# Performance work log

Measured on AMD Instinct MI355X. Metric: run time of the kernel, lower is better.

The kernel has to match this reference:

```python
import jax, jax.numpy as jnp
import numpy as np

B, T, N, F = 8, 24, 207, 16
H = 64            # hidden_dim
DH = 16           # dims_hyper[-1] / node-embedding out
DA = 4 * F        # temporal attention dim_out
DS = 64           # ss_gal gcn out dim (last_ss_gal_dim)
GDEP = 2
ALPHA, BETA, GAMMA = 0.05, 0.95, 0.95
TA = 2.0


def _lin(x, w, b=None):
    y = x @ w
    return y if b is None else y + b


def gcn_hyper(x, A, W, b):
    # x: [B,N,C], A: [N,N] static. h <- a*x + g * einsum('nvc,vw->nwc', h, A)
    h = x
    outs = [h]
    for _ in range(GDEP):
        h = ALPHA * x + GAMMA * jnp.einsum('bvc,vw->bwc', h, A)
        outs.append(h)
    return _lin(jnp.concatenate(outs, axis=-1), W, b)


def gcn_gru(x, A_dyn, A_sta, W, b):
    # x: [B,N,C], A_dyn: [B,N,N], A_sta: [N,N]
    h = x
    outs = [h]
    for _ in range(GDEP):
        h = (ALPHA * x
             + BETA * jnp.einsum('bvw,bvc->bwc', A_dyn, h)     # bmm(A^T, h)
             + GAMMA * jnp.einsum('bvc,vw->bwc', h, A_sta))
        outs.append(h)
    return _lin(jnp.concatenate(outs, axis=-1), W, b)


def gcn_ssgal(x, A, W, b):
    # x: [B*,N,C], A: [B*,N,N]
    h = x
    outs = [h]
    for _ in range(GDEP):
        h = ALPHA * x + GAMMA * jnp.einsum('bvw,bvc->bwc', A, h)
        outs.append(h)
    return _lin(jnp.concatenate(outs, axis=-1), W, b)


def setup_inputs() -> dict:
    key = jax.random.key(0)
    ks = jax.random.split(key, 32)
    i = iter(range(32))
    w = lambda *s: (0.02 * jax.random.normal(ks[next(i)], s, dtype=jnp.float32))
    inp = {
        'input_sequence': jax.random.normal(ks[next(i)], (B, T, N, F), dtype=jnp.float32),
        'static_adj': jax.random.uniform(ks[next(i)], (N, N), dtype=jnp.float32),
        # hyper graph generators: mlp in = (GDEP+1)*H -> DH
        'src_gen_w': w((GDEP + 1) * H, DH), 'src_gen_b': w(DH),
        'tgt_gen_w': w((GDEP + 1) * H, DH), 'tgt_gen_b': w(DH),
        # node embeddings: F -> DH
        'src_emb_w': w(F, DH), 'src_emb_b': w(DH),
        'tgt_emb_w': w(F, DH), 'tgt_emb_b': w(DH),
        # GRU gate GCNs: mlp in = (GDEP+1)*(F+H) -> H
        'gru_z_w': w((GDEP + 1) * (F + H), H), 'gru_z_b': w(H),
        'gru_r_w': w((GDEP + 1) * (F + H), H), 'gru_r_b': w(H),
        'gru_c_w': w((GDEP + 1) * (F + H), H), 'gru_c_b': w(H),
        # temporal attention: F -> DA, score DA -> 1
        'attn_q_w': w(F, DA),
        'attn_k_w': w(F, DA), 'attn_k_b': w(DA),
        'attn_s_w': w(DA, 1),
        # ss_gal spatial gcn: (GDEP+1)*F -> DS
        'sgcn_w': w((GDEP + 1) * F, DS), 'sgcn_b': w(DS),
        # predictors
        'short_w': w(DS, F), 'short_b': w(F),
        'long_w': w(H, F), 'long_b': w(F),
        'fus_w': w(DS + H, F), 'fus_b': w(F),
    }
    return inp


def _forward(input_sequence, static_adj,
             src_gen_w, src_gen_b, tgt_gen_w, tgt_gen_b,
             src_emb_w, src_emb_b, tgt_emb_w, tgt_emb_b,
             gru_z_w, gru_z_b, gru_r_w, gru_r_b, gru_c_w, gru_c_b,
             attn_q_w, attn_k_w, attn_k_b, attn_s_w,
             sgcn_w, sgcn_b,
             short_w, short_b, long_w, long_b, fus_w, fus_b):
    batch, steps, nodes = input_sequence.shape[0], input_sequence.shape[1], input_sequence.shape[2]
    eye = jnp.eye(nodes, dtype=input_sequence.dtype)

    def cell(x_t, h):
        # x_t: [B,N,F], h: [B,N,H]
        src_ctx = gcn_hyper(h, static_adj, src_gen_w, src_gen_b)   # [B,N,DH]
        tgt_ctx = gcn_hyper(h, static_adj, tgt_gen_w, tgt_gen_b)
        s = jnp.tanh(TA * _lin(x_t, src_emb_w, src_emb_b) * src_ctx)
        t = jnp.tanh(TA * _lin(x_t, tgt_emb_w, tgt_emb_b) * tgt_ctx)
        asym = jnp.einsum('bnc,bmc->bnm', s, t) - jnp.einsum('bnc,bmc->bnm', t, s)
        adj = jax.nn.relu(jnp.tanh(TA * asym)) + eye
        adj = adj / (adj.sum(axis=-1, keepdims=True) + 1e-8)
        gi = jnp.concatenate([x_t, h], axis=-1)
        z = jax.nn.sigmoid(gcn_gru(gi, adj, static_adj, gru_z_w, gru_z_b))
        r = jax.nn.sigmoid(gcn_gru(gi, adj, static_adj, gru_r_w, gru_r_b))
        ri = jnp.concatenate([x_t, r * h], axis=-1)
        c = jnp.tanh(gcn_gru(ri, adj, static_adj, gru_c_w, gru_c_b))
        return z * h + (1.0 - z) * c

    h = jnp.zeros((batch, nodes, H), dtype=input_sequence.dtype)
    for t_step in range(0, max(1, steps - 4), 4):
        h = cell(input_sequence[:, t_step], h)

    # ss_gal branch on the last 4 steps
    recent = input_sequence[:, -4:]            # [B,4,N,F]
    target = input_sequence[:, -1]             # [B,N,F]
    # temporal attention
    q = target @ attn_q_w                      # [B,N,DA]
    k = recent @ attn_k_w + attn_k_b           # [B,4,N,DA]
    scores = jnp.tanh(q[:, None, :, None, :] + k[:, :, None, :, :])  # [B,4,N,N,DA]
    scores = jnp.squeeze(scores @ attn_s_w, axis=-1)                  # [B,4,N,N]
    attn = jax.nn.softmax(scores, axis=-1)
    dyn_adj = static_adj[None] + attn.reshape(-1, nodes, nodes)       # [B*4,N,N]
    rh = recent.reshape(-1, nodes, recent.shape[-1])                  # [B*4,N,F]
    rh = gcn_ssgal(rh, dyn_adj, sgcn_w, sgcn_b)                       # [B*4,N,DS]
    rh = jax.nn.relu(rh.reshape(batch, -1, nodes, rh.shape[-1]))      # [B,4,N,DS]
    target = jnp.sum(rh, axis=1)                                       # [B,N,DS]

    short = _lin(target, short_w, short_b)      # [B,N,F]
    h = cell(short, h)                          # final GRU step on short-term prediction
    long = _lin(h, long_w, long_b)              # [B,N,F]
    fused = _lin(jnp.concatenate([target, h], axis=-1), fus_w, fus_b)  # [B,N,F]
    return jnp.stack([short, long, fused], axis=0)  # [3,B,N,F]


def reference(input_sequence, static_adj,
              src_gen_w, src_gen_b, tgt_gen_w, tgt_gen_b,
              src_emb_w, src_emb_b, tgt_emb_w, tgt_emb_b,
              gru_z_w, gru_z_b, gru_r_w, gru_r_b, gru_c_w, gru_c_b,
              attn_q_w, attn_k_w, attn_k_b, attn_s_w,
              sgcn_w, sgcn_b,
              short_w, short_b, long_w, long_b, fus_w, fus_b):
    return _forward(input_sequence, static_adj,
                    src_gen_w, src_gen_b, tgt_gen_w, tgt_gen_b,
                    src_emb_w, src_emb_b, tgt_emb_w, tgt_emb_b,
                    gru_z_w, gru_z_b, gru_r_w, gru_r_b, gru_c_w, gru_c_b,
                    attn_q_w, attn_k_w, attn_k_b, attn_s_w,
                    sgcn_w, sgcn_b,
                    short_w, short_b, long_w, long_b, fus_w, fus_b)
```

## Files before the change

kernel.cpp:

```cpp
#include <hip/hip_runtime.h>


constexpr int B = 8, T = 24, N = 207, F = 16, H = 64, DH = 16;
constexpr int PS = 208;
constexpr float ALPHA = 0.05f, BETA = 0.95f, GAMMA = 0.95f, TA = 2.0f;
constexpr int NF = N * F;
constexpr int BNF = B * N * F;

__device__ __forceinline__ float tanh_fast(float x) { float e = __expf(2.f * x); return 1.f - 2.f / (e + 1.f); }
__device__ __forceinline__ float sigm(float x) { return 1.f / (1.f + __expf(-x)); }
__device__ __forceinline__ float tanh_pade(float x) {
    float x2 = x * x;
    float p = x * (27.f + x2);
    float q = 27.f + 9.f * x2;
    float r = p * __builtin_amdgcn_rcpf(q);
    return fminf(1.f, fmaxf(-1.f, r));
}

__global__ __launch_bounds__(256) void k_build_Ts(const float* __restrict__ adj, float* __restrict__ Ts) {
    int i = blockIdx.x * 256 + threadIdx.x;
    if (i >= N * N) return;
    int w = i / N, v = i % N;
    Ts[(size_t)w * PS + v] = adj[v * N + w];
}

__global__ __launch_bounds__(256) void k_mm_sq(const float* __restrict__ Ain, float* __restrict__ Aout) {
    int bb = blockIdx.z;
    const float* A = Ain + (size_t)bb * PS * PS;
    float* O = Aout + (size_t)bb * PS * PS;
    int w0 = blockIdx.x * 32, v0 = blockIdx.y * 32;
    int tid = threadIdx.x;
    __shared__ float sA[32][33], sB[32][33];
    float acc[4] = {0, 0, 0, 0};
    int i0 = tid >> 5, j = tid & 31;
    int r = tid >> 3, c4 = (tid & 7) * 4;
    for (int u0 = 0; u0 < N; u0 += 32) {
        float4 av = {0, 0, 0, 0}, bv = {0, 0, 0, 0};
        int w = w0 + r, u = u0 + r;
        if (w < N) av = *(const float4*)&A[(size_t)w * PS + u0 + c4];
        if (u < N) bv = *(const float4*)&A[(size_t)u * PS + v0 + c4];
        __syncthreads();
        sA[r][c4] = av.x; sA[r][c4 + 1] = av.y; sA[r][c4 + 2] = av.z; sA[r][c4 + 3] = av.w;
        sB[r][c4] = bv.x; sB[r][c4 + 1] = bv.y; sB[r][c4 + 2] = bv.z; sB[r][c4 + 3] = bv.w;
        __syncthreads();
#pragma unroll 8
        for (int u_ = 0; u_ < 32; u_++) {
            float bvv = sB[u_][j];
#pragma unroll
            for (int k = 0; k < 4; k++) acc[k] += sA[i0 + k * 8][u_] * bvv;
        }
    }
#pragma unroll
    for (int k = 0; k < 4; k++) {
        int w = w0 + i0 + k * 8, v = v0 + j;
        if (w < N && v < N) O[(size_t)w * PS + v] = acc[k];
    }
}

__global__ __launch_bounds__(256) void k_cell_a(
    const float* __restrict__ h, const float* __restrict__ Ts, const float* __restrict__ A2,
    const float* __restrict__ xseq, int tsel, const float* __restrict__ xbuf,
    const float* __restrict__ Wsrc, const float* __restrict__ bsrc,
    const float* __restrict__ Wtgt, const float* __restrict__ btgt,
    const float* __restrict__ Wes, const float* __restrict__ bes,
    const float* __restrict__ Wet, const float* __restrict__ bet,
    float* __restrict__ s_out, float* __restrict__ t_out, float* __restrict__ catg) {
    int b = blockIdx.y, w0 = blockIdx.x * 16;
    int tid = threadIdx.x, ty = tid >> 4, tx = tid & 15;
    __shared__ float sTs[16][33], sA2[16][33];
    __shared__ float sH[32][64];
    __shared__ float cat[16][193];
    __shared__ float sW[192][16];
    __shared__ float sX[16][16], sWe[16][16];
    float au[4] = {0, 0, 0, 0}, aw[4] = {0, 0, 0, 0};
    const float* hb = h + b * N * H;
    const float* xp = (tsel >= 0) ? (xseq + ((size_t)(b * T + tsel)) * NF) : (xbuf + (size_t)b * NF);
    int pidx = tid & 127;
    int pr = pidx >> 3, pc4 = (pidx & 7) * 4;
    for (int v0 = 0; v0 < N; v0 += 32) {
        float4 t4 = {0, 0, 0, 0};
        {
            const float* src = (tid < 128) ? Ts : A2;
            int w = w0 + pr;
            if (w < N) t4 = *(const float4*)&src[(size_t)w * PS + v0 + pc4];
        }
        float4 h4[2];
        int hr[2], hc[2];
#pragma unroll
        for (int k = 0; k < 2; k++) {
            int l4 = tid + k * 256;
            hr[k] = l4 >> 4; hc[k] = (l4 & 15) * 4;
            float4 hv = {0, 0, 0, 0};
            int v = v0 + hr[k];
            if (v < N) hv = *(const float4*)&hb[(size_t)v * H + hc[k]];
            h4[k] = hv;
        }
        __syncthreads();
        {
            float (*dst)[33] = (tid < 128) ? sTs : sA2;
            dst[pr][pc4] = t4.x; dst[pr][pc4 + 1] = t4.y; dst[pr][pc4 + 2] = t4.z; dst[pr][pc4 + 3] = t4.w;
        }
#pragma unroll
        for (int k = 0; k < 2; k++) *(float4*)&sH[hr[k]][hc[k]] = h4[k];
        __syncthreads();
#pragma unroll 8
        for (int v = 0; v < 32; v++) {
            float pu = sTs[ty][v], pw = sA2[ty][v];
#pragma unroll
            for (int j = 0; j < 4; j++) {
                float x = sH[v][tx * 4 + j];
                au[j] += pu * x; aw[j] += pw * x;
            }
        }
    }
    int w = w0 + ty;
    bool valid = w < N;
    __syncthreads();
    if (valid) {
#pragma unroll
        for (int j = 0; j < 4; j++) {
            int c = tx * 4 + j;
            float hv = hb[w * H + c];
            float u = au[j], w2 = aw[j];
            cat[ty][c] = hv;
            cat[ty][64 + c] = ALPHA * hv + GAMMA * u;
            cat[ty][128 + c] = ALPHA * hv + ALPHA * GAMMA * u + GAMMA * GAMMA * w2;
        }
    } else {
#pragma unroll
        for (int j = 0; j < 4; j++) {
            int c = tx * 4 + j;
            cat[ty][c] = 0; cat[ty][64 + c] = 0; cat[ty][128 + c] = 0;
        }
    }
    {
        float4 wv[3];
#pragma unroll
        for (int k = 0; k < 3; k++) {
            int l4 = tid + k * 256;
            wv[k] = *(const float4*)&Wsrc[l4 * 4];
        }
        float4 xv = {0, 0, 0, 0}, ev = {0, 0, 0, 0};
        int sr = 0, sc = 0;
        if (tid < 64) {
            sr = tid >> 2; sc = (tid & 3) * 4;
            int n = w0 + sr;
            if (n < N) xv = *(const float4*)&xp[(size_t)n * F + sc];
            ev = *(const float4*)&Wes[tid * 4];
        }
#pragma unroll
        for (int k = 0; k < 3; k++) {
            int l4 = tid + k * 256;
            int r = l4 >> 2, c4 = (l4 & 3) * 4;
            *(float4*)&sW[r][c4] = wv[k];
        }
        if (tid < 64) {
            *(float4*)&sX[sr][sc] = xv;
            *(float4*)&sWe[sr][sc] = ev;
        }
    }
    __syncthreads();
    if (valid) {
#pragma unroll
        for (int j = 0; j < 5; j++) {
            int c = tx * 5 + j;
            float v = (c < 16) ? sX[ty][c] : hb[w * H + (c - 16)];
            catg[((size_t)(b * N + w)) * 240 + c] = v;
        }
    }
    {
        float ctx = bsrc[tx];
#pragma unroll 8
        for (int c = 0; c < 192; c++) ctx += cat[ty][c] * sW[c][tx];
        float xe = bes[tx];
#pragma unroll
        for (int f = 0; f < 16; f++) xe += sX[ty][f] * sWe[f][tx];
        if (valid) s_out[(b * N + w) * DH + tx] = tanh_fast(TA * xe * ctx);
    }
    __syncthreads();
    {
        float4 wv[3];
#pragma unroll
        for (int k = 0; k < 3; k++) {
            int l4 = tid + k * 256;
            wv[k] = *(const float4*)&Wtgt[l4 * 4];
        }
        float4 ev = {0, 0, 0, 0};
        if (tid < 64) ev = *(const float4*)&Wet[tid * 4];
#pragma unroll
        for (int k = 0; k < 3; k++) {
            int l4 = tid + k * 256;
            int r = l4 >> 2, c4 = (l4 & 3) * 4;
            *(float4*)&sW[r][c4] = wv[k];
        }
        if (tid < 64) *(float4*)&sWe[tid >> 2][(tid & 3) * 4] = ev;
    }
    __syncthreads();
    {
        float ctx = btgt[tx];
#pragma unroll 8
        for (int c = 0; c < 192; c++) ctx += cat[ty][c] * sW[c][tx];
        float xe = bet[tx];
#pragma unroll
        for (int f = 0; f < 16; f++) xe += sX[ty][f] * sWe[f][tx];
        if (valid) t_out[(b * N + w) * DH + tx] = tanh_fast(TA * xe * ctx);
    }
}

__global__ __launch_bounds__(256) void k_cell_bP(const float* __restrict__ s_in, const float* __restrict__ t_in,
                                                 const float* __restrict__ adj, float* __restrict__ P) {
    int b = blockIdx.y, v0 = blockIdx.x * 16;
    int tid = threadIdx.x, ty = tid >> 4, tx = tid & 15;
    __shared__ float sS[N][17], sT[N][17];
    for (int l4 = tid; l4 < 828; l4 += 256) {
        float4 sv = *(const float4*)&s_in[(size_t)b * N * 16 + l4 * 4];
        float4 tv = *(const float4*)&t_in[(size_t)b * N * 16 + l4 * 4];
        int r = l4 >> 2, c = (l4 & 3) * 4;
        sS[r][c] = sv.x; sS[r][c + 1] = sv.y; sS[r][c + 2] = sv.z; sS[r][c + 3] = sv.w;
        sT[r][c] = tv.x; sT[r][c + 1] = tv.y; sT[r][c + 2] = tv.z; sT[r][c + 3] = tv.w;
    }
    __syncthreads();
    int v = v0 + ty;
    bool valid = v < N;
    int vc = valid ? v : (N - 1);
    float sv[16], tv[16];
#pragma unroll
    for (int k = 0; k < 16; k++) { sv[k] = sS[vc][k]; tv[k] = sT[vc][k]; }
    float val[13];
    float rsum = 0.f;
#pragma unroll
    for (int idx = 0; idx < 13; idx++) {
        int w = tx + 16 * idx;
        float r = 0.f;
        if (w < N) {
            float a = 0.f;
#pragma unroll
            for (int k = 0; k < 16; k++) a += sv[k] * sT[w][k] - tv[k] * sS[w][k];
            r = tanh_fast(TA * a);
            r = r > 0.f ? r : 0.f;
            if (w == v) r += 1.f;
        }
        val[idx] = r;
        rsum += r;
    }
    float tot = rsum;
    for (int d = 8; d > 0; d >>= 1) tot += __shfl_down(tot, d, 16);
    tot = __shfl(tot, 0, 16);
    float rinv = BETA / (tot + 1e-8f);
    if (valid) {
        float* Pb = P + (size_t)b * PS * PS;
#pragma unroll
        for (int idx = 0; idx < 13; idx++) {
            int w = tx + 16 * idx;
            if (w < N) Pb[(size_t)w * PS + v] = val[idx] * rinv + GAMMA * adj[v * N + w];
        }
    }
}

__global__ __launch_bounds__(256) void k_combineT(const float* __restrict__ Ain, const float* __restrict__ rs,
                                                  const float* __restrict__ Ts, float* __restrict__ Pout,
                                                  float cA, float cT) {
    int bt = blockIdx.z;
    int w0 = blockIdx.x * 32, v0 = blockIdx.y * 32;
    int tid = threadIdx.x;
    __shared__ float tile[32][33];
    __shared__ float rsv[32];
    int r = tid >> 3, c4 = (tid & 7) * 4;
    float4 a4 = {0, 0, 0, 0};
    int v = v0 + r;
    if (v < N) a4 = *(const float4*)&Ain[(size_t)bt * PS * PS + (size_t)v * PS + w0 + c4];
    tile[r][c4] = a4.x; tile[r][c4 + 1] = a4.y; tile[r][c4 + 2] = a4.z; tile[r][c4 + 3] = a4.w;
    if (tid < 32) {
        int vv = v0 + tid;
        rsv[tid] = (vv < N) ? (cA / rs[bt * N + vv]) : 0.f;
    }
    __syncthreads();
    for (int l = tid; l < 1024; l += 256) {
        int i = l >> 5, j = l & 31;
        int w = w0 + i, vv = v0 + j;
        if (w < N && vv < N)
            Pout[(size_t)bt * PS * PS + (size_t)w * PS + vv] = tile[j][i] * rsv[j] + cT * Ts[(size_t)w * PS + vv];
    }
}

__global__ __launch_bounds__(256) void k_prop2(const float* __restrict__ P, const float* __restrict__ P2,
                                               float* __restrict__ cat) {
    int b = blockIdx.y, w0 = blockIdx.x * 16, c0 = blockIdx.z * 16;
    int tid = threadIdx.x, ty = tid >> 4, tx = tid & 15;
    const float* Pb = P + (size_t)b * PS * PS;
    const float* P2b = P2 + (size_t)b * PS * PS;
    __shared__ float sP[16][33], sP2[16][33], sX[32][17];
    float a1 = 0.f, a2 = 0.f;
    int pr = tid >> 4, pc = (tid & 15) * 2;
    int xr = tid >> 3, xc = (tid & 7) * 2;
    for (int v0 = 0; v0 < N; v0 += 32) {
        float2 pv = {0, 0}, p2v = {0, 0}, xv = {0, 0};
        int w = w0 + pr;
        if (w < N) {
            pv = *(const float2*)&Pb[(size_t)w * PS + v0 + pc];
            p2v = *(const float2*)&P2b[(size_t)w * PS + v0 + pc];
        }
        int vv = v0 + xr;
        if (vv < N) xv = *(const float2*)&cat[((size_t)(b * N + vv)) * 240 + c0 + xc];
        __syncthreads();
        sP[pr][pc] = pv.x; sP[pr][pc + 1] = pv.y;
        sP2[pr][pc] = p2v.x; sP2[pr][pc + 1] = p2v.y;
        sX[xr][xc] = xv.x; sX[xr][xc + 1] = xv.y;
        __syncthreads();
#pragma unroll 8
        for (int v_ = 0; v_ < 32; v_++) {
            float xx = sX[v_][tx];
            a1 += sP[ty][v_] * xx;
            a2 += sP2[ty][v_] * xx;
        }
    }
    int w = w0 + ty, c = c0 + tx;
    if (w < N) {
        size_t base = ((size_t)(b * N + w)) * 240;
        float x0 = cat[base + c];
        cat[base + 80 + c] = ALPHA * x0 + a1;
        cat[base + 160 + c] = ALPHA * x0 + ALPHA * a1 + a2;
    }
}

__global__ __launch_bounds__(256) void k_gate(
    const float* __restrict__ cat,
    const float* __restrict__ Wa, const float* __restrict__ ba,
    const float* __restrict__ Wb, const float* __restrict__ bb,
    int baseMode,
    const float* __restrict__ xseq, int tsel, const float* __restrict__ xbuf,
    float* __restrict__ zbuf, float* __restrict__ ricat,
    float* __restrict__ h,
    const float* __restrict__ target,
    const float* __restrict__ Wlong, const float* __restrict__ blong,
    const float* __restrict__ Wfus, const float* __restrict__ bfus,
    float* __restrict__ out) {
    int mode = baseMode + blockIdx.z;
    const float* W = (mode == 1) ? Wb : Wa;
    const float* bias = (mode == 1) ? bb : ba;
    int b = blockIdx.y, w0 = blockIdx.x * 16;
    int tid = threadIdx.x, ty = tid >> 4, tx = tid & 15;
    __shared__ float sC[16][241];
    __shared__ float sW[48][65];
    __shared__ float hrow[16][65], trow[16][65];
    for (int l4 = tid; l4 < 960; l4 += 256) {
        int r = l4 / 60, cc = (l4 % 60) * 4;
        int w = w0 + r;
        float4 v4 = {0, 0, 0, 0};
        if (w < N) v4 = *(const float4*)&cat[((size_t)(b * N + w)) * 240 + cc];
        sC[r][cc] = v4.x; sC[r][cc + 1] = v4.y; sC[r][cc + 2] = v4.z; sC[r][cc + 3] = v4.w;
    }
    float acc[4];
#pragma unroll
    for (int j = 0; j < 4; j++) acc[j] = bias[tx * 4 + j];
    for (int c0 = 0; c0 < 240; c0 += 48) {
        float4 wv[3];
#pragma unroll
        for (int k = 0; k < 3; k++) {
            int l4 = tid + k * 256;
            wv[k] = *(const float4*)&W[(size_t)c0 * 64 + l4 * 4];
        }
        __syncthreads();
#pragma unroll
        for (int k = 0; k < 3; k++) {
            int l4 = tid + k * 256;
            int r = l4 >> 4, cc = (l4 & 15) * 4;
            sW[r][cc] = wv[k].x; sW[r][cc + 1] = wv[k].y; sW[r][cc + 2] = wv[k].z; sW[r][cc + 3] = wv[k].w;
        }
        __syncthreads();
#pragma unroll 8
        for (int cc = 0; cc < 48; cc++) {
            float cv = sC[ty][c0 + cc];
#pragma unroll
            for (int j = 0; j < 4; j++) acc[j] += cv * sW[cc][tx * 4 + j];
        }
    }
    int w = w0 + ty;
    bool valid = w < N;
    if (mode == 0) {
        if (valid) {
#pragma unroll
            for (int j = 0; j < 4; j++) zbuf[((size_t)(b * N + w)) * 64 + tx * 4 + j] = sigm(acc[j]);
        }
    } else if (mode == 1) {
        if (valid) {
#pragma unroll
            for (int j = 0; j < 4; j++) {
                int o = tx * 4 + j;
                ricat[((size_t)(b * N + w)) * 240 + 16 + o] = sigm(acc[j]) * h[((size_t)(b * N + w)) * 64 + o];
            }
            if (tx < 4) {
                const float* xp = (tsel >= 0) ? (xseq + ((size_t)(b * T + tsel)) * NF) : (xbuf + (size_t)b * NF);
#pragma unroll
                for (int j = 0; j < 4; j++) {
                    int c = tx * 4 + j;
                    ricat[((size_t)(b * N + w)) * 240 + c] = xp[w * F + c];
                }
            }
        }
    } else {
#pragma unroll
        for (int j = 0; j < 4; j++) {
            int o = tx * 4 + j;
            float cval = tanh_fast(acc[j]);
            float zv = 0.f, hv = 0.f;
            if (valid) { zv = zbuf[((size_t)(b * N + w)) * 64 + o]; hv = h[((size_t)(b * N + w)) * 64 + o]; }
            float hn = zv * hv + (1.f - zv) * cval;
            if (valid) h[((size_t)(b * N + w)) * 64 + o] = hn;
            hrow[ty][o] = valid ? hn : 0.f;
        }
        if (mode == 3) {
            for (int l = tid; l < 1024; l += 256) {
                int i = l >> 6, o = l & 63;
                int ww = w0 + i;
                trow[i][o] = (ww < N) ? target[((size_t)(b * N + ww)) * 64 + o] : 0.f;
            }
            __syncthreads();
            float lg = blong[tx];
            float fs = bfus[tx];
            for (int o = 0; o < 64; o++) {
                lg += hrow[ty][o] * Wlong[o * 16 + tx];
                fs += trow[ty][o] * Wfus[o * 16 + tx] + hrow[ty][o] * Wfus[(64 + o) * 16 + tx];
            }
            if (valid) {
                out[((size_t)1 * B * N + b * N + w) * 16 + tx] = lg;
                out[((size_t)2 * B * N + b * N + w) * 16 + tx] = fs;
            }
        }
    }
}

__global__ __launch_bounds__(256) void k_qk(const float* __restrict__ inp,
                                            const float* __restrict__ Wq,
                                            const float* __restrict__ Wk,
                                            const float* __restrict__ kb,
                                            float* __restrict__ q, float* __restrict__ kkk) {
    int b = blockIdx.z, which = blockIdx.y, n0 = blockIdx.x * 16;
    int tid = threadIdx.x, ty = tid >> 4, tx = tid & 15;
    __shared__ float sX[16][16], sW[16][64];
    int tsel = (which == 0) ? (T - 1) : (T - 4 + which - 1);
    const float* W = (which == 0) ? Wq : Wk;
    {
        float4 wv = *(const float4*)&W[tid * 4];
        float4 xv = {0, 0, 0, 0};
        if (tid < 64) {
            int r = tid >> 2, c4 = (tid & 3) * 4;
            int n = n0 + r;
            if (n < N) xv = *(const float4*)&inp[((size_t)(b * T + tsel) * N + n) * F + c4];
            *(float4*)&sX[r][c4] = xv;
        }
        *(float4*)&sW[tid >> 4][(tid & 15) * 4] = wv;
    }
    __syncthreads();
    float acc[4];
#pragma unroll
    for (int j = 0; j < 4; j++) {
        int o = tx * 4 + j;
        float a = (which == 0) ? 0.f : kb[o];
        for (int f = 0; f < 16; f++) a += sX[ty][f] * sW[f][o];
        acc[j] = a;
    }
    int n = n0 + ty;
    if (n < N) {
        float* dst = (which == 0) ? (q + (b * N + n) * 64) : (kkk + ((b * 4 + (which - 1)) * N + n) * 64);
#pragma unroll
        for (int j = 0; j < 4; j++) dst[tx * 4 + j] = acc[j];
    }
}

__global__ __launch_bounds__(256) void k_attn2(const float* __restrict__ q, const float* __restrict__ kkk,
                                               const float* __restrict__ sw_,
                                               float* __restrict__ attnU, float* __restrict__ rsum) {
    int bt = blockIdx.z, b = bt >> 2;
    int n0 = blockIdx.x * 16, m0 = blockIdx.y * 16;
    int tid = threadIdx.x, ti = tid >> 4, tj = tid & 15;
    __shared__ float sQ[16][65], sK[16][65], ssw[64];
    {
        int r = tid >> 4, c4 = (tid & 15) * 4;
        int n = n0 + r, m = m0 + r;
        float4 qv = {0, 0, 0, 0}, kv = {0, 0, 0, 0};
        if (n < N) qv = *(const float4*)&q[((size_t)(b * N + n)) * 64 + c4];
        if (m < N) kv = *(const float4*)&kkk[((size_t)(bt * N + m)) * 64 + c4];
        sQ[r][c4] = qv.x; sQ[r][c4 + 1] = qv.y; sQ[r][c4 + 2] = qv.z; sQ[r][c4 + 3] = qv.w;
        sK[r][c4] = kv.x; sK[r][c4 + 1] = kv.y; sK[r][c4 + 2] = kv.z; sK[r][c4 + 3] = kv.w;
    }
    if (tid < 64) ssw[tid] = sw_[tid];
    __syncthreads();
    float sc = 0.f;
#pragma unroll 4
    for (int d = 0; d < 64; d++) sc += tanh_pade(sQ[ti][d] + sK[tj][d]) * ssw[d];
    int n = n0 + ti, m = m0 + tj;
    bool vn = n < N, vm = m < N;
    float e = (vn && vm) ? __expf(sc) : 0.f;
    float part = e;
    for (int d = 8; d > 0; d >>= 1) part += __shfl_down(part, d, 16);
    if (tj == 0 && vn) atomicAdd(&rsum[bt * N + n], part);
    if (vn && vm) attnU[(size_t)bt * PS * PS + (size_t)n * PS + m] = e;
}

__global__ __launch_bounds__(256) void k_prop_xr(const float* __restrict__ Pd, const float* __restrict__ inp,
                                                 float* __restrict__ x1) {
    int bt = blockIdx.y, w0 = blockIdx.x * 16;
    int b = bt >> 2, tau = bt & 3;
    const float* xb = inp + ((size_t)(b * T + 20 + tau)) * NF;
    const float* Pb = Pd + (size_t)bt * PS * PS;
    int tid = threadIdx.x, ty = tid >> 4, tx = tid & 15;
    __shared__ float sP[16][33];
    __shared__ float sX[32][17];
    float acc = 0.f;
    for (int v0 = 0; v0 < N; v0 += 32) {
        float4 pv = {0, 0, 0, 0}, xv = {0, 0, 0, 0};
        if (tid < 128) {
            int r = tid >> 3, c4 = (tid & 7) * 4;
            int w = w0 + r;
            if (w < N) pv = *(const float4*)&Pb[(size_t)w * PS + v0 + c4];
        } else {
            int idx = tid - 128;
            int r = idx >> 2, c4 = (idx & 3) * 4;
            int v = v0 + r;
            if (v < N) xv = *(const float4*)&xb[(size_t)v * F + c4];
        }
        __syncthreads();
        if (tid < 128) {
            int r = tid >> 3, c4 = (tid & 7) * 4;
            sP[r][c4] = pv.x; sP[r][c4 + 1] = pv.y; sP[r][c4 + 2] = pv.z; sP[r][c4 + 3] = pv.w;
        } else {
            int idx = tid - 128;
            int r = idx >> 2, c4 = (idx & 3) * 4;
            sX[r][c4] = xv.x; sX[r][c4 + 1] = xv.y; sX[r][c4 + 2] = xv.z; sX[r][c4 + 3] = xv.w;
        }
        __syncthreads();
#pragma unroll 8
        for (int v = 0; v < 32; v++) acc += sP[ty][v] * sX[v][tx];
    }
    int w = w0 + ty;
    if (w < N) x1[((size_t)(bt * N + w)) * 16 + tx] = ALPHA * xb[w * F + tx] + acc;
}

__global__ __launch_bounds__(256) void k_sgc2(const float* __restrict__ Pd, const float* __restrict__ x1,
                                              const float* __restrict__ inp,
                                              const float* __restrict__ Ws, const float* __restrict__ bs,
                                              float* __restrict__ target) {
    int bt = blockIdx.y, b = bt >> 2, tau = bt & 3, w0 = blockIdx.x * 16;
    const float* xb = inp + ((size_t)(b * T + 20 + tau)) * NF;
    const float* Pb = Pd + (size_t)bt * PS * PS;
    int tid = threadIdx.x, ty = tid >> 4, tx = tid & 15;
    __shared__ float sP[16][33], sX[32][17], cat[16][48], sW[48][64];
    float acc = 0.f;
    for (int v0 = 0; v0 < N; v0 += 32) {
        float4 pv = {0, 0, 0, 0}, xv = {0, 0, 0, 0};
        if (tid < 128) {
            int r = tid >> 3, c4 = (tid & 7) * 4;
            int w = w0 + r;
            if (w < N) pv = *(const float4*)&Pb[(size_t)w * PS + v0 + c4];
        } else {
            int idx = tid - 128;
            int r = idx >> 2, c4 = (idx & 3) * 4;
            int v = v0 + r;
            if (v < N) xv = *(const float4*)&x1[((size_t)(bt * N + v)) * 16 + c4];
        }
        __syncthreads();
        if (tid < 128) {
            int r = tid >> 3, c4 = (tid & 7) * 4;
            sP[r][c4] = pv.x; sP[r][c4 + 1] = pv.y; sP[r][c4 + 2] = pv.z; sP[r][c4 + 3] = pv.w;
        } else {
            int idx = tid - 128;
            int r = idx >> 2, c4 = (idx & 3) * 4;
            sX[r][c4] = xv.x; sX[r][c4 + 1] = xv.y; sX[r][c4 + 2] = xv.z; sX[r][c4 + 3] = xv.w;
        }
        __syncthreads();
#pragma unroll 8
        for (int v = 0; v < 32; v++) acc += sP[ty][v] * sX[v][tx];
    }
    int w = w0 + ty;
    bool valid = w < N;
    __syncthreads();
    for (int l = tid; l < 512; l += 256) {
        int i = l >> 5, c = l & 31;
        int ww = w0 + i;
        float vv = 0;
        if (ww < N) {
            if (c < 16) vv = xb[ww * F + c];
            else vv = x1[((size_t)bt * N + ww) * 16 + (c - 16)];
        }
        cat[i][c] = vv;
    }
    {
        float x0 = valid ? xb[w * F + tx] : 0.f;
        cat[ty][32 + tx] = ALPHA * x0 + acc;
    }
    {
        float4 wv[3];
#pragma unroll
        for (int k = 0; k < 3; k++) wv[k] = *(const float4*)&Ws[(tid + k * 256) * 4];
#pragma unroll
        for (int k = 0; k < 3; k++) {
            int l4 = tid + k * 256;
            *(float4*)&sW[l4 >> 4][(l4 & 15) * 4] = wv[k];
        }
    }
    __syncthreads();
    float a[4];
#pragma unroll
    for (int j = 0; j < 4; j++) a[j] = bs[tx * 4 + j];
#pragma unroll 8
    for (int cc = 0; cc < 48; cc++) {
        float cv = cat[ty][cc];
#pragma unroll
        for (int j = 0; j < 4; j++) a[j] += cv * sW[cc][tx * 4 + j];
    }
    if (valid) {
#pragma unroll
        for (int j = 0; j < 4; j++) {
            float r = a[j] > 0.f ? a[j] : 0.f;
            atomicAdd(&target[(b * N + w) * 64 + tx * 4 + j], r);
        }
    }
}

__global__ __launch_bounds__(256) void k_short(const float* __restrict__ target,
                                               const float* __restrict__ Wsh, const float* __restrict__ bsh,
                                               float* __restrict__ out, float* __restrict__ xshort) {
    int b = blockIdx.y, n0 = blockIdx.x * 16;
    int tid = threadIdx.x, ty = tid >> 4, tx = tid & 15;
    __shared__ float trow[16][65], sW[64][16];
    {
        int r = tid >> 4, c4 = (tid & 15) * 4;
        int n = n0 + r;
        float4 tv = {0, 0, 0, 0};
        if (n < N) tv = *(const float4*)&target[((size_t)(b * N + n)) * 64 + c4];
        trow[r][c4] = tv.x; trow[r][c4 + 1] = tv.y; trow[r][c4 + 2] = tv.z; trow[r][c4 + 3] = tv.w;
        float4 wv = *(const float4*)&Wsh[tid * 4];
        *(float4*)&sW[tid >> 2][(tid & 3) * 4] = wv;
    }
    __syncthreads();
    float a = bsh[tx];
#pragma unroll 8
    for (int o = 0; o < 64; o++) a += trow[ty][o] * sW[o][tx];
    int n = n0 + ty;
    if (n < N) {
        out[((size_t)0 * B * N + b * N + n) * 16 + tx] = a;
        xshort[(b * N + n) * 16 + tx] = a;
    }
}

extern "C" void kernel_launch(void* const* d_in, const int* in_sizes, int n_in,
                              void* d_out, int out_size, void* d_ws, size_t ws_size,
                              hipStream_t stream) {
    const float* inp = (const float*)d_in[0];
    const float* adj = (const float*)d_in[1];
    const float* src_gen_w = (const float*)d_in[2];
    const float* src_gen_b = (const float*)d_in[3];
    const float* tgt_gen_w = (const float*)d_in[4];
    const float* tgt_gen_b = (const float*)d_in[5];
    const float* src_emb_w = (const float*)d_in[6];
    const float* src_emb_b = (const float*)d_in[7];
    const float* tgt_emb_w = (const float*)d_in[8];
    const float* tgt_emb_b = (const float*)d_in[9];
    const float* gru_z_w = (const float*)d_in[10];
    const float* gru_z_b = (const float*)d_in[11];
    const float* gru_r_w = (const float*)d_in[12];
    const float* gru_r_b = (const float*)d_in[13];
    const float* gru_c_w = (const float*)d_in[14];
    const float* gru_c_b = (const float*)d_in[15];
    const float* attn_q_w = (const float*)d_in[16];
    const float* attn_k_w = (const float*)d_in[17];
    const float* attn_k_b = (const float*)d_in[18];
    const float* attn_s_w = (const float*)d_in[19];
    const float* sgcn_w = (const float*)d_in[20];
    const float* sgcn_b = (const float*)d_in[21];
    const float* short_w = (const float*)d_in[22];
    const float* short_b = (const float*)d_in[23];
    const float* long_w = (const float*)d_in[24];
    const float* long_b = (const float*)d_in[25];
    const float* fus_w = (const float*)d_in[26];
    const float* fus_b = (const float*)d_in[27];
    float* out = (float*)d_out;

    float* ws = (float*)d_ws;
    size_t off = 0;
    auto A = [&](size_t n) { n = (n + 3) & ~(size_t)3; float* p = ws + off; off += n; return p; };
    float* Ts = A((size_t)PS * PS);
    float* A2 = A((size_t)PS * PS);
    float* h = A((size_t)B * N * H);
    float* sbuf = A((size_t)B * N * DH);
    float* tbuf = A((size_t)B * N * DH);
    float* P = A((size_t)B * PS * PS);
    float* P2 = A((size_t)B * PS * PS);
    float* catg = A((size_t)B * N * 240);
    float* catc = A((size_t)B * N * 240);
    float* zb = A((size_t)B * N * 64);
    float* q = A((size_t)B * N * 64);
    float* kk = A((size_t)B * 4 * N * 64);
    float* attnU = A((size_t)32 * PS * PS);
    float* Pd = A((size_t)32 * PS * PS);
    float* x1 = A((size_t)32 * NF);
    float* target = A((size_t)B * N * 64);
    float* rsum = A((size_t)32 * N);
    float* xshort = A(BNF);
    (void)ws_size; (void)in_sizes; (void)n_in; (void)out_size;

    hipMemsetAsync(h, 0, sizeof(float) * B * N * H, stream);
    hipMemsetAsync(target, 0, sizeof(float) * (B * N * 64), stream);
    hipMemsetAsync(rsum, 0, sizeof(float) * (32 * N), stream);
    k_build_Ts<<<(N * N + 255) / 256, 256, 0, stream>>>(adj, Ts);
    k_mm_sq<<<dim3(7, 7, 1), 256, 0, stream>>>(Ts, A2);

    auto run_cell = [&](int tsel, const float* xbuf, int finalFlag) {
        k_cell_a<<<dim3(13, B), 256, 0, stream>>>(h, Ts, A2, inp, tsel, xbuf,
                                                  src_gen_w, src_gen_b, tgt_gen_w, tgt_gen_b,
                                                  src_emb_w, src_emb_b, tgt_emb_w, tgt_emb_b, sbuf, tbuf, catg);
        k_cell_bP<<<dim3(13, B), 256, 0, stream>>>(sbuf, tbuf, adj, P);
        k_mm_sq<<<dim3(7, 7, B), 256, 0, stream>>>(P, P2);
        k_prop2<<<dim3(13, B, 5), 256, 0, stream>>>(P, P2, catg);
        k_gate<<<dim3(13, B, 2), 256, 0, stream>>>(catg, gru_z_w, gru_z_b, gru_r_w, gru_r_b, 0,
                                                   inp, tsel, xbuf, zb, catc, h,
                                                   nullptr, nullptr, nullptr, nullptr, nullptr, nullptr);
        k_prop2<<<dim3(13, B, 5), 256, 0, stream>>>(P, P2, catc);
        k_gate<<<dim3(13, B, 1), 256, 0, stream>>>(catc, gru_c_w, gru_c_b, nullptr, nullptr, 2 + finalFlag,
                                                   nullptr, 0, nullptr, zb, nullptr, h,
                                                   target, long_w, long_b, fus_w, fus_b, out);
    };

    for (int t = 0; t < 20; t += 4) run_cell(t, nullptr, 0);

    k_qk<<<dim3(13, 5, B), 256, 0, stream>>>(inp, attn_q_w, attn_k_w, attn_k_b, q, kk);
    k_attn2<<<dim3(13, 13, 32), 256, 0, stream>>>(q, kk, attn_s_w, attnU, rsum);
    k_combineT<<<dim3(7, 7, 32), 256, 0, stream>>>(attnU, rsum, Ts, Pd, GAMMA, GAMMA);
    k_prop_xr<<<dim3(13, 32), 256, 0, stream>>>(Pd, inp, x1);
    k_sgc2<<<dim3(13, 32), 256, 0, stream>>>(Pd, x1, inp, sgcn_w, sgcn_b, target);
    k_short<<<dim3(13, B), 256, 0, stream>>>(target, short_w, short_b, out, xshort);

    run_cell(-1, xshort, 1);
}
```

Before: 728.0 us.

## Double-buffer shared-memory tiles in GEMM-like kernels and fuse Q/K projection into attention

Converts the tiled loops in k_mm_sq, k_cell_a, k_prop2, k_gate, k_prop_xr and k_sgc2 to double-buffered shared memory. Each thread issues the global loads for the next tile before computing on the current one, so load latency overlaps with the FMA loop. It also drops the separate k_qk launch and its q/kk buffers by computing the Q and K projections inside k_attn2 from the input. This removes one launch and a global round trip, but recomputes the projections redundantly in each attention block and increases LDS use per block.

```diff
diff --git a/kernel.cpp b/kernel.cpp
--- a/kernel.cpp
+++ b/kernel.cpp
@@ -28,31 +28,38 @@
     int bb = blockIdx.z;
     const float* A = Ain + (size_t)bb * PS * PS;
     float* O = Aout + (size_t)bb * PS * PS;
-    int w0 = blockIdx.x * 32, v0 = blockIdx.y * 32;
+    int w0 = blockIdx.x * 32, v0b = blockIdx.y * 32;
     int tid = threadIdx.x;
-    __shared__ float sA[32][33], sB[32][33];
+    __shared__ float sA[2][32][33], sB[2][32][33];
     float acc[4] = {0, 0, 0, 0};
     int i0 = tid >> 5, j = tid & 31;
     int r = tid >> 3, c4 = (tid & 7) * 4;
-    for (int u0 = 0; u0 < N; u0 += 32) {
-        float4 av = {0, 0, 0, 0}, bv = {0, 0, 0, 0};
+    float4 av, bv;
+    auto loadT = [&](int u0) {
+        av = make_float4(0, 0, 0, 0); bv = make_float4(0, 0, 0, 0);
         int w = w0 + r, u = u0 + r;
         if (w < N) av = *(const float4*)&A[(size_t)w * PS + u0 + c4];
-        if (u < N) bv = *(const float4*)&A[(size_t)u * PS + v0 + c4];
-        __syncthreads();
-        sA[r][c4] = av.x; sA[r][c4 + 1] = av.y; sA[r][c4 + 2] = av.z; sA[r][c4 + 3] = av.w;
-        sB[r][c4] = bv.x; sB[r][c4 + 1] = bv.y; sB[r][c4 + 2] = bv.z; sB[r][c4 + 3] = bv.w;
+        if (u < N) bv = *(const float4*)&A[(size_t)u * PS + v0b + c4];
+    };
+    loadT(0);
+    int cur = 0;
+    for (int t = 0; t < 7; t++) {
+        __syncthreads();
+        sA[cur][r][c4] = av.x; sA[cur][r][c4 + 1] = av.y; sA[cur][r][c4 + 2] = av.z; sA[cur][r][c4 + 3] = av.w;
+        sB[cur][r][c4] = bv.x; sB[cur][r][c4 + 1] = bv.y; sB[cur][r][c4 + 2] = bv.z; sB[cur][r][c4 + 3] = bv.w;
+        if (t < 6) loadT((t + 1) * 32);
         __syncthreads();
 #pragma unroll 8
         for (int u_ = 0; u_ < 32; u_++) {
-            float bvv = sB[u_][j];
-#pragma unroll
-            for (int k = 0; k < 4; k++) acc[k] += sA[i0 + k * 8][u_] * bvv;
-        }
+            float bvv = sB[cur][u_][j];
+#pragma unroll
+            for (int k = 0; k < 4; k++) acc[k] += sA[cur][i0 + k * 8][u_] * bvv;
+        }
+        cur ^= 1;
     }
 #pragma unroll
     for (int k = 0; k < 4; k++) {
-        int w = w0 + i0 + k * 8, v = v0 + j;
+        int w = w0 + i0 + k * 8, v = v0b + j;
         if (w < N && v < N) O[(size_t)w * PS + v] = acc[k];
     }
 }
@@ -67,8 +74,8 @@
     float* __restrict__ s_out, float* __restrict__ t_out, float* __restrict__ catg) {
     int b = blockIdx.y, w0 = blockIdx.x * 16;
     int tid = threadIdx.x, ty = tid >> 4, tx = tid & 15;
-    __shared__ float sTs[16][33], sA2[16][33];
-    __shared__ float sH[32][64];
+    __shared__ float sTs[2][16][33], sA2[2][16][33];
+    __shared__ float sH[2][32][64];
     __shared__ float cat[16][193];
     __shared__ float sW[192][16];
     __shared__ float sX[16][16], sWe[16][16];
@@ -77,41 +84,46 @@
     const float* xp = (tsel >= 0) ? (xseq + ((size_t)(b * T + tsel)) * NF) : (xbuf + (size_t)b * NF);
     int pidx = tid & 127;
     int pr = pidx >> 3, pc4 = (pidx & 7) * 4;
-    for (int v0 = 0; v0 < N; v0 += 32) {
-        float4 t4 = {0, 0, 0, 0};
-        {
-            const float* src = (tid < 128) ? Ts : A2;
-            int w = w0 + pr;
-            if (w < N) t4 = *(const float4*)&src[(size_t)w * PS + v0 + pc4];
-        }
-        float4 h4[2];
-        int hr[2], hc[2];
+    float4 t4;
+    float4 h4[2];
+    int hr[2], hc[2];
+#pragma unroll
+    for (int k = 0; k < 2; k++) { int l4 = tid + k * 256; hr[k] = l4 >> 4; hc[k] = (l4 & 15) * 4; }
+    auto loadT = [&](int v0) {
+        t4 = make_float4(0, 0, 0, 0);
+        const float* src = (tid < 128) ? Ts : A2;
+        int w = w0 + pr;
+        if (w < N) t4 = *(const float4*)&src[(size_t)w * PS + v0 + pc4];
 #pragma unroll
         for (int k = 0; k < 2; k++) {
-            int l4 = tid + k * 256;
-            hr[k] = l4 >> 4; hc[k] = (l4 & 15) * 4;
-            float4 hv = {0, 0, 0, 0};
+            float4 hv = make_float4(0, 0, 0, 0);
             int v = v0 + hr[k];
             if (v < N) hv = *(const float4*)&hb[(size_t)v * H + hc[k]];
             h4[k] = hv;
         }
+    };
+    loadT(0);
+    int cur = 0;
+    for (int t = 0; t < 7; t++) {
         __syncthreads();
         {
-            float (*dst)[33] = (tid < 128) ? sTs : sA2;
+            float (*dst)[33] = (tid < 128) ? sTs[cur] : sA2[cur];
             dst[pr][pc4] = t4.x; dst[pr][pc4 + 1] = t4.y; dst[pr][pc4 + 2] = t4.z; dst[pr][pc4 + 3] = t4.w;
         }
 #pragma unroll
-        for (int k = 0; k < 2; k++) *(float4*)&sH[hr[k]][hc[k]] = h4[k];
+        for (int k = 0; k < 2; k++) *(float4*)&sH[cur][hr[k]][hc[k]] = h4[k];
+        if (t < 6) loadT((t + 1) * 32);
         __syncthreads();
 #pragma unroll 8
         for (int v = 0; v < 32; v++) {
-            float pu = sTs[ty][v], pw = sA2[ty][v];
+            float pu = sTs[cur][ty][v], pw = sA2[cur][ty][v];
 #pragma unroll
             for (int j = 0; j < 4; j++) {
-                float x = sH[v][tx * 4 + j];
+                float x = sH[cur][v][tx * 4 + j];
                 au[j] += pu * x; aw[j] += pw * x;
             }
         }
+        cur ^= 1;
     }
     int w = w0 + ty;
     bool valid = w < N;
@@ -140,7 +152,7 @@
             int l4 = tid + k * 256;
             wv[k] = *(const float4*)&Wsrc[l4 * 4];
         }
-        float4 xv = {0, 0, 0, 0}, ev = {0, 0, 0, 0};
+        float4 xv = make_float4(0, 0, 0, 0), ev = make_float4(0, 0, 0, 0);
         int sr = 0, sc = 0;
         if (tid < 64) {
             sr = tid >> 2; sc = (tid & 3) * 4;
@@ -185,7 +197,7 @@
             int l4 = tid + k * 256;
             wv[k] = *(const float4*)&Wtgt[l4 * 4];
         }
-        float4 ev = {0, 0, 0, 0};
+        float4 ev = make_float4(0, 0, 0, 0);
         if (tid < 64) ev = *(const float4*)&Wet[tid * 4];
 #pragma unroll
         for (int k = 0; k < 3; k++) {
@@ -266,7 +278,7 @@
     __shared__ float tile[32][33];
     __shared__ float rsv[32];
     int r = tid >> 3, c4 = (tid & 7) * 4;
-    float4 a4 = {0, 0, 0, 0};
+    float4 a4 = make_float4(0, 0, 0, 0);
     int v = v0 + r;
     if (v < N) a4 = *(const float4*)&Ain[(size_t)bt * PS * PS + (size_t)v * PS + w0 + c4];
     tile[r][c4] = a4.x; tile[r][c4 + 1] = a4.y; tile[r][c4 + 2] = a4.z; tile[r][c4 + 3] = a4.w;
@@ -289,12 +301,13 @@
     int tid = threadIdx.x, ty = tid >> 4, tx = tid & 15;
     const float* Pb = P + (size_t)b * PS * PS;
     const float* P2b = P2 + (size_t)b * PS * PS;
-    __shared__ float sP[16][33], sP2[16][33], sX[32][17];
+    __shared__ float sP[2][16][33], sP2[2][16][33], sX[2][32][17];
     float a1 = 0.f, a2 = 0.f;
     int pr = tid >> 4, pc = (tid & 15) * 2;
     int xr = tid >> 3, xc = (tid & 7) * 2;
-    for (int v0 = 0; v0 < N; v0 += 32) {
-        float2 pv = {0, 0}, p2v = {0, 0}, xv = {0, 0};
+    float2 pv, p2v, xv;
+    auto loadT = [&](int v0) {
+        pv = make_float2(0, 0); p2v = make_float2(0, 0); xv = make_float2(0, 0);
         int w = w0 + pr;
         if (w < N) {
             pv = *(const float2*)&Pb[(size_t)w * PS + v0 + pc];
@@ -302,17 +315,23 @@
         }
         int vv = v0 + xr;
         if (vv < N) xv = *(const float2*)&cat[((size_t)(b * N + vv)) * 240 + c0 + xc];
-        __syncthreads();
-        sP[pr][pc] = pv.x; sP[pr][pc + 1] = pv.y;
-        sP2[pr][pc] = p2v.x; sP2[pr][pc + 1] = p2v.y;
-        sX[xr][xc] = xv.x; sX[xr][xc + 1] = xv.y;
+    };
+    loadT(0);
+    int cur = 0;
+    for (int t = 0; t < 7; t++) {
+        __syncthreads();
+        sP[cur][pr][pc] = pv.x; sP[cur][pr][pc + 1] = pv.y;
+        sP2[cur][pr][pc] = p2v.x; sP2[cur][pr][pc + 1] = p2v.y;
+        sX[cur][xr][xc] = xv.x; sX[cur][xr][xc + 1] = xv.y;
+        if (t < 6) loadT((t + 1) * 32);
         __syncthreads();
 #pragma unroll 8
         for (int v_ = 0; v_ < 32; v_++) {
-            float xx = sX[v_][tx];
-            a1 += sP[ty][v_] * xx;
-            a2 += sP2[ty][v_] * xx;
-        }
+            float xx = sX[cur][v_][tx];
+            a1 += sP[cur][ty][v_] * xx;
+            a2 += sP2[cur][ty][v_] * xx;
+        }
+        cur ^= 1;
     }
     int w = w0 + ty, c = c0 + tx;
     if (w < N) {
@@ -341,39 +360,43 @@
     int b = blockIdx.y, w0 = blockIdx.x * 16;
     int tid = threadIdx.x, ty = tid >> 4, tx = tid & 15;
     __shared__ float sC[16][241];
-    __shared__ float sW[48][65];
+    __shared__ float sW[2][48][65];
     __shared__ float hrow[16][65], trow[16][65];
     for (int l4 = tid; l4 < 960; l4 += 256) {
         int r = l4 / 60, cc = (l4 % 60) * 4;
         int w = w0 + r;
-        float4 v4 = {0, 0, 0, 0};
+        float4 v4 = make_float4(0, 0, 0, 0);
         if (w < N) v4 = *(const float4*)&cat[((size_t)(b * N + w)) * 240 + cc];
         sC[r][cc] = v4.x; sC[r][cc + 1] = v4.y; sC[r][cc + 2] = v4.z; sC[r][cc + 3] = v4.w;
     }
     float acc[4];
 #pragma unroll
     for (int j = 0; j < 4; j++) acc[j] = bias[tx * 4 + j];
-    for (int c0 = 0; c0 < 240; c0 += 48) {
-        float4 wv[3];
-#pragma unroll
-        for (int k = 0; k < 3; k++) {
-            int l4 = tid + k * 256;
-            wv[k] = *(const float4*)&W[(size_t)c0 * 64 + l4 * 4];
-        }
+    float4 wv[3];
+#pragma unroll
+    for (int k = 0; k < 3; k++) wv[k] = *(const float4*)&W[(tid + k * 256) * 4];
+    int cur = 0;
+    for (int ch = 0; ch < 5; ch++) {
         __syncthreads();
 #pragma unroll
         for (int k = 0; k < 3; k++) {
             int l4 = tid + k * 256;
             int r = l4 >> 4, cc = (l4 & 15) * 4;
-            sW[r][cc] = wv[k].x; sW[r][cc + 1] = wv[k].y; sW[r][cc + 2] = wv[k].z; sW[r][cc + 3] = wv[k].w;
-        }
-        __syncthreads();
+            sW[cur][r][cc] = wv[k].x; sW[cur][r][cc + 1] = wv[k].y; sW[cur][r][cc + 2] = wv[k].z; sW[cur][r][cc + 3] = wv[k].w;
+        }
+        if (ch < 4) {
+#pragma unroll
+            for (int k = 0; k < 3; k++) wv[k] = *(const float4*)&W[(size_t)(ch + 1) * 48 * 64 + (tid + k * 256) * 4];
+        }
+        __syncthreads();
+        int c0 = ch * 48;
 #pragma unroll 8
         for (int cc = 0; cc < 48; cc++) {
             float cv = sC[ty][c0 + cc];
 #pragma unroll
-            for (int j = 0; j < 4; j++) acc[j] += cv * sW[cc][tx * 4 + j];
-        }
+            for (int j = 0; j < 4; j++) acc[j] += cv * sW[cur][cc][tx * 4 + j];
+        }
+        cur ^= 1;
     }
     int w = w0 + ty;
     bool valid = w < N;
@@ -430,61 +453,47 @@
     }
 }
 
-__global__ __launch_bounds__(256) void k_qk(const float* __restrict__ inp,
-                                            const float* __restrict__ Wq,
-                                            const float* __restrict__ Wk,
-                                            const float* __restrict__ kb,
-                                            float* __restrict__ q, float* __restrict__ kkk) {
-    int b = blockIdx.z, which = blockIdx.y, n0 = blockIdx.x * 16;
-    int tid = threadIdx.x, ty = tid >> 4, tx = tid & 15;
-    __shared__ float sX[16][16], sW[16][64];
-    int tsel = (which == 0) ? (T - 1) : (T - 4 + which - 1);
-    const float* W = (which == 0) ? Wq : Wk;
-    {
-        float4 wv = *(const float4*)&W[tid * 4];
-        float4 xv = {0, 0, 0, 0};
-        if (tid < 64) {
-            int r = tid >> 2, c4 = (tid & 3) * 4;
-            int n = n0 + r;
-            if (n < N) xv = *(const float4*)&inp[((size_t)(b * T + tsel) * N + n) * F + c4];
-            *(float4*)&sX[r][c4] = xv;
-        }
-        *(float4*)&sW[tid >> 4][(tid & 15) * 4] = wv;
-    }
-    __syncthreads();
-    float acc[4];
-#pragma unroll
-    for (int j = 0; j < 4; j++) {
-        int o = tx * 4 + j;
-        float a = (which == 0) ? 0.f : kb[o];
-        for (int f = 0; f < 16; f++) a += sX[ty][f] * sW[f][o];
-        acc[j] = a;
-    }
-    int n = n0 + ty;
-    if (n < N) {
-        float* dst = (which == 0) ? (q + (b * N + n) * 64) : (kkk + ((b * 4 + (which - 1)) * N + n) * 64);
-#pragma unroll
-        for (int j = 0; j < 4; j++) dst[tx * 4 + j] = acc[j];
-    }
-}
-
-__global__ __launch_bounds__(256) void k_attn2(const float* __restrict__ q, const float* __restrict__ kkk,
-                                               const float* __restrict__ sw_,
+__global__ __launch_bounds__(256) void k_attn2(const float* __restrict__ inp,
+                                               const float* __restrict__ Wq, const float* __restrict__ Wk,
+                                               const float* __restrict__ kb, const float* __restrict__ sw_,
                                                float* __restrict__ attnU, float* __restrict__ rsum) {
-    int bt = blockIdx.z, b = bt >> 2;
+    int bt = blockIdx.z, b = bt >> 2, tau = bt & 3;
     int n0 = blockIdx.x * 16, m0 = blockIdx.y * 16;
     int tid = threadIdx.x, ti = tid >> 4, tj = tid & 15;
-    __shared__ float sQ[16][65], sK[16][65], ssw[64];
-    {
-        int r = tid >> 4, c4 = (tid & 15) * 4;
-        int n = n0 + r, m = m0 + r;
-        float4 qv = {0, 0, 0, 0}, kv = {0, 0, 0, 0};
-        if (n < N) qv = *(const float4*)&q[((size_t)(b * N + n)) * 64 + c4];
-        if (m < N) kv = *(const float4*)&kkk[((size_t)(bt * N + m)) * 64 + c4];
-        sQ[r][c4] = qv.x; sQ[r][c4 + 1] = qv.y; sQ[r][c4 + 2] = qv.z; sQ[r][c4 + 3] = qv.w;
-        sK[r][c4] = kv.x; sK[r][c4 + 1] = kv.y; sK[r][c4 + 2] = kv.z; sK[r][c4 + 3] = kv.w;
-    }
-    if (tid < 64) ssw[tid] = sw_[tid];
+    __shared__ float sQ[16][65], sK[16][65];
+    __shared__ float sWq[16][64], sWk[16][64];
+    __shared__ float sXq[16][16], sXk[16][16];
+    __shared__ float ssw[64], skb[64];
+    const float* xq = inp + ((size_t)(b * T + (T - 1))) * NF;
+    const float* xk = inp + ((size_t)(b * T + 20 + tau)) * NF;
+    {
+        float4 wq4 = *(const float4*)&Wq[tid * 4];
+        float4 wk4 = *(const float4*)&Wk[tid * 4];
+        *(float4*)&sWq[tid >> 4][(tid & 15) * 4] = wq4;
+        *(float4*)&sWk[tid >> 4][(tid & 15) * 4] = wk4;
+        if (tid < 64) { ssw[tid] = sw_[tid]; skb[tid] = kb[tid]; }
+        if (tid >= 64 && tid < 128) {
+            int idx = tid - 64;
+            int r = idx >> 2, c4 = (idx & 3) * 4;
+            int n = n0 + r, m = m0 + r;
+            float4 a = make_float4(0, 0, 0, 0), c = make_float4(0, 0, 0, 0);
+            if (n < N) a = *(const float4*)&xq[(size_t)n * F + c4];
+            if (m < N) c = *(const float4*)&xk[(size_t)m * F + c4];
+            *(float4*)&sXq[r][c4] = a;
+            *(float4*)&sXk[r][c4] = c;
+        }
+    }
+    __syncthreads();
+    {
+#pragma unroll
+        for (int j = 0; j < 4; j++) {
+            int o = tj * 4 + j;
+            float aq = 0.f, ak = skb[o];
+#pragma unroll
+            for (int f = 0; f < 16; f++) { aq += sXq[ti][f] * sWq[f][o]; ak += sXk[ti][f] * sWk[f][o]; }
+            sQ[ti][o] = aq; sK[ti][o] = ak;
+        }
+    }
     __syncthreads();
     float sc = 0.f;
 #pragma unroll 4
@@ -505,33 +514,36 @@
     const float* xb = inp + ((size_t)(b * T + 20 + tau)) * NF;
     const float* Pb = Pd + (size_t)bt * PS * PS;
     int tid = threadIdx.x, ty = tid >> 4, tx = tid & 15;
-    __shared__ float sP[16][33];
-    __shared__ float sX[32][17];
+    __shared__ float sP[2][16][33];
+    __shared__ float sX[2][32][17];
     float acc = 0.f;
-    for (int v0 = 0; v0 < N; v0 += 32) {
-        float4 pv = {0, 0, 0, 0}, xv = {0, 0, 0, 0};
+    int prr = tid >> 3, pcc = (tid & 7) * 4;
+    int xrr = (tid - 128) >> 2, xcc = ((tid - 128) & 3) * 4;
+    float4 pv, xv;
+    auto loadT = [&](int v0) {
+        pv = make_float4(0, 0, 0, 0); xv = make_float4(0, 0, 0, 0);
         if (tid < 128) {
-            int r = tid >> 3, c4 = (tid & 7) * 4;
-            int w = w0 + r;
-            if (w < N) pv = *(const float4*)&Pb[(size_t)w * PS + v0 + c4];
+            int w = w0 + prr;
+            if (w < N) pv = *(const float4*)&Pb[(size_t)w * PS + v0 + pcc];
         } else {
-            int idx = tid - 128;
-            int r = idx >> 2, c4 = (idx & 3) * 4;
-            int v = v0 + r;
-            if (v < N) xv = *(const float4*)&xb[(size_t)v * F + c4];
-        }
+            int v = v0 + xrr;
+            if (v < N) xv = *(const float4*)&xb[(size_t)v * F + xcc];
+        }
+    };
+    loadT(0);
+    int cur = 0;
+    for (int t = 0; t < 7; t++) {
         __syncthreads();
         if (tid < 128) {
-            int r = tid >> 3, c4 = (tid & 7) * 4;
-            sP[r][c4] = pv.x; sP[r][c4 + 1] = pv.y; sP[r][c4 + 2] = pv.z; sP[r][c4 + 3] = pv.w;
+            sP[cur][prr][pcc] = pv.x; sP[cur][prr][pcc + 1] = pv.y; sP[cur][prr][pcc + 2] = pv.z; sP[cur][prr][pcc + 3] = pv.w;
         } else {
-            int idx = tid - 128;
-            int r = idx >> 2, c4 = (idx & 3) * 4;
-            sX[r][c4] = xv.x; sX[r][c4 + 1] = xv.y; sX[r][c4 + 2] = xv.z; sX[r][c4 + 3] = xv.w;
-        }
-        __syncthreads();
-#pragma unroll 8
-        for (int v = 0; v < 32; v++) acc += sP[ty][v] * sX[v][tx];
+            sX[cur][xrr][xcc] = xv.x; sX[cur][xrr][xcc + 1] = xv.y; sX[cur][xrr][xcc + 2] = xv.z; sX[cur][xrr][xcc + 3] = xv.w;
+        }
+        if (t < 6) loadT((t + 1) * 32);
+        __syncthreads();
+#pragma unroll 8
+        for (int v = 0; v < 32; v++) acc += sP[cur][ty][v] * sX[cur][v][tx];
+        cur ^= 1;
     }
     int w = w0 + ty;
     if (w < N) x1[((size_t)(bt * N + w)) * 16 + tx] = ALPHA * xb[w * F + tx] + acc;
@@ -545,32 +557,35 @@
     const float* xb = inp + ((size_t)(b * T + 20 + tau)) * NF;
     const float* Pb = Pd + (size_t)bt * PS * PS;
     int tid = threadIdx.x, ty = tid >> 4, tx = tid & 15;
-    __shared__ float sP[16][33], sX[32][17], cat[16][48], sW[48][64];
+    __shared__ float sP[2][16][33], sX[2][32][17], cat[16][48], sW[48][64];
     float acc = 0.f;
-    for (int v0 = 0; v0 < N; v0 += 32) {
-        float4 pv = {0, 0, 0, 0}, xv = {0, 0, 0, 0};
+    int prr = tid >> 3, pcc = (tid & 7) * 4;
+    int xrr = (tid - 128) >> 2, xcc = ((tid - 128) & 3) * 4;
+    float4 pv, xv;
+    auto loadT = [&](int v0) {
+        pv = make_float4(0, 0, 0, 0); xv = make_float4(0, 0, 0, 0);
         if (tid < 128) {
-            int r = tid >> 3, c4 = (tid & 7) * 4;
-            int w = w0 + r;
-            if (w < N) pv = *(const float4*)&Pb[(size_t)w * PS + v0 + c4];
+            int w = w0 + prr;
+            if (w < N) pv = *(const float4*)&Pb[(size_t)w * PS + v0 + pcc];
         } else {
-            int idx = tid - 128;
-            int r = idx >> 2, c4 = (idx & 3) * 4;
-            int v = v0 + r;
-            if (v < N) xv = *(const float4*)&x1[((size_t)(bt * N + v)) * 16 + c4];
-        }
+            int v = v0 + xrr;
+            if (v < N) xv = *(const float4*)&x1[((size_t)(bt * N + v)) * 16 + xcc];
+        }
+    };
+    loadT(0);
+    int cur = 0;
+    for (int t = 0; t < 7; t++) {
         __syncthreads();
         if (tid < 128) {
-            int r = tid >> 3, c4 = (tid & 7) * 4;
-            sP[r][c4] = pv.x; sP[r][c4 + 1] = pv.y; sP[r][c4 + 2] = pv.z; sP[r][c4 + 3] = pv.w;
+            sP[cur][prr][pcc] = pv.x; sP[cur][prr][pcc + 1] = pv.y; sP[cur][prr][pcc + 2] = pv.z; sP[cur][prr][pcc + 3] = pv.w;
         } else {
-            int idx = tid - 128;
-            int r = idx >> 2, c4 = (idx & 3) * 4;
-            sX[r][c4] = xv.x; sX[r][c4 + 1] = xv.y; sX[r][c4 + 2] = xv.z; sX[r][c4 + 3] = xv.w;
-        }
-        __syncthreads();
-#pragma unroll 8
-        for (int v = 0; v < 32; v++) acc += sP[ty][v] * sX[v][tx];
+            sX[cur][xrr][xcc] = xv.x; sX[cur][xrr][xcc + 1] = xv.y; sX[cur][xrr][xcc + 2] = xv.z; sX[cur][xrr][xcc + 3] = xv.w;
+        }
+        if (t < 6) loadT((t + 1) * 32);
+        __syncthreads();
+#pragma unroll 8
+        for (int v = 0; v < 32; v++) acc += sP[cur][ty][v] * sX[cur][v][tx];
+        cur ^= 1;
     }
     int w = w0 + ty;
     bool valid = w < N;
@@ -627,7 +642,7 @@
     {
         int r = tid >> 4, c4 = (tid & 15) * 4;
         int n = n0 + r;
-        float4 tv = {0, 0, 0, 0};
+        float4 tv = make_float4(0, 0, 0, 0);
         if (n < N) tv = *(const float4*)&target[((size_t)(b * N + n)) * 64 + c4];
         trow[r][c4] = tv.x; trow[r][c4 + 1] = tv.y; trow[r][c4 + 2] = tv.z; trow[r][c4 + 3] = tv.w;
         float4 wv = *(const float4*)&Wsh[tid * 4];
@@ -690,8 +705,6 @@
     float* catg = A((size_t)B * N * 240);
     float* catc = A((size_t)B * N * 240);
     float* zb = A((size_t)B * N * 64);
-    float* q = A((size_t)B * N * 64);
-    float* kk = A((size_t)B * 4 * N * 64);
     float* attnU = A((size_t)32 * PS * PS);
     float* Pd = A((size_t)32 * PS * PS);
     float* x1 = A((size_t)32 * NF);
@@ -724,8 +737,7 @@
 
     for (int t = 0; t < 20; t += 4) run_cell(t, nullptr, 0);
 
-    k_qk<<<dim3(13, 5, B), 256, 0, stream>>>(inp, attn_q_w, attn_k_w, attn_k_b, q, kk);
-    k_attn2<<<dim3(13, 13, 32), 256, 0, stream>>>(q, kk, attn_s_w, attnU, rsum);
+    k_attn2<<<dim3(13, 13, 32), 256, 0, stream>>>(inp, attn_q_w, attn_k_w, attn_k_b, attn_s_w, attnU, rsum);
     k_combineT<<<dim3(7, 7, 32), 256, 0, stream>>>(attnU, rsum, Ts, Pd, GAMMA, GAMMA);
     k_prop_xr<<<dim3(13, 32), 256, 0, stream>>>(Pd, inp, x1);
     k_sgc2<<<dim3(13, 32), 256, 0, stream>>>(Pd, x1, inp, sgcn_w, sgcn_b, target);
```

Result: faster. 702.2 us (-3.6%).
